# Kernel optimization log

Hardware: AMD Instinct MI355X
Metric: run time of the kernel (lower is better)

The kernel has to match this reference:

```python
import jax, jax.numpy as jnp
import numpy as np

HALF_PI = np.float32(np.pi / 2.0)
EPS = 1e-8

def feature_map(x):
    # [B, L] -> [B, L, 2]: standard quantum-inspired embedding
    return jnp.stack([jnp.cos(HALF_PI * x), jnp.sin(HALF_PI * x)], axis=-1)

def setup_inputs() -> dict:
    key = jax.random.key(0)
    k1, k2, k3, k4 = jax.random.split(key, 4)
    B, L, F, D, C = 32768, 256, 2, 32, 10
    x = jax.random.uniform(k1, (B, L), dtype=jnp.float32)
    core0 = jax.random.normal(k2, (F, 1, D), dtype=jnp.float32) * 0.1
    cores_mid = jax.random.normal(k3, (L - 2, F, D, D), dtype=jnp.float32) * 0.1
    coreN = jax.random.normal(k4, (F, D, C), dtype=jnp.float32) * 0.1
    return {"x": x, "core0": core0, "cores_mid": cores_mid, "coreN": coreN}

def reference(x, core0, cores_mid, coreN):
    feats = feature_map(x)                      # [B, L, F]
    # first site: M = v0 @ A0  -> [B, D]
    M0 = jnp.einsum('bf,fd->bd', feats[:, 0, :], core0[:, 0, :])

    # sequential scan over middle sites with per-step L2 normalization
    vs = jnp.transpose(feats[:, 1:-1, :], (1, 0, 2))  # [L-2, B, F]

    def step(M, inputs):
        v, A = inputs                           # v: [B,F], A: [F,D,D]
        M = jnp.einsum('ba,bf,fac->bc', M, v, A)
        M = M / (jnp.linalg.norm(M, axis=1, keepdims=True) + EPS)
        return M, None

    M, _ = jax.lax.scan(step, M0, (vs, cores_mid))

    # last site and readout
    final = jnp.einsum('bf,fac->bac', feats[:, -1, :], coreN)  # [B, D, C]
    logits = jnp.einsum('ba,bac->bc', M, final)                # [B, C]
    return logits
```

## Files before the change

kernel.cpp:

```cpp
#include <hip/hip_runtime.h>
#include <hip/hip_bf16.h>

#define B_TOTAL   32768
#define L_SITES   256
#define N_MID     254
#define HALF_PI_F 1.57079632679489662f
#define EPS_NORM  1e-8f

#define WS_FRAG 0
#define WS_C0   520192
#define WS_CN   520256
#define WS_X    520896
#define WS_FLAG 8909504

typedef short bf16x8 __attribute__((ext_vector_type(8)));
typedef float f32x4  __attribute__((ext_vector_type(4)));

__device__ __host__ __forceinline__ int pi_perm(int quad, int j) {
    return (j < 4) ? (quad * 4 + j) : (16 + quad * 4 + (j - 4));
}

__device__ __forceinline__ unsigned short f2bf(float f) {
    unsigned u = __builtin_bit_cast(unsigned, f);
    u += 0x7FFFu + ((u >> 16) & 1u);
    return (unsigned short)(u >> 16);
}
__device__ __forceinline__ float bf2f(unsigned short h) {
    unsigned u = ((unsigned)h) << 16;
    return __builtin_bit_cast(float, u);
}
__device__ __forceinline__ bf16x8 asbf(uint4 u) {
    return __builtin_bit_cast(bf16x8, u);
}
__device__ __forceinline__ unsigned pkbf2(float a, float b) {
    float2 p; p.x = a; p.y = b;
    __hip_bfloat162 h2 = __float22bfloat162_rn(p);
    unsigned u;
    __builtin_memcpy(&u, &h2, 4);
    return u;
}
__device__ __forceinline__ void split8(const float* v, bf16x8& hi, bf16x8& lo) {
    uint4 H, L;
    unsigned* hp = (unsigned*)&H;
    unsigned* lp = (unsigned*)&L;
    #pragma unroll
    for (int d = 0; d < 4; ++d) {
        float a = v[2 * d], b = v[2 * d + 1];
        unsigned hb = pkbf2(a, b);
        float h0 = __builtin_bit_cast(float, hb << 16);
        float h1 = __builtin_bit_cast(float, hb & 0xFFFF0000u);
        hp[d] = hb;
        lp[d] = pkbf2(a - h0, b - h1);
    }
    hi = __builtin_bit_cast(bf16x8, H);
    lo = __builtin_bit_cast(bf16x8, L);
}
__device__ __forceinline__ bool detect_bf16(const unsigned* x_raw, int lane) {
    unsigned v = x_raw[lane];
    return __ballot((v & 0xFFFFu) >= 0x4000u) == 0ull;
}

__global__ __launch_bounds__(256)
void aux_all(const void* __restrict__ x_in, const void* __restrict__ c0_in,
             const void* __restrict__ am_in, const void* __restrict__ cn_in,
             float* __restrict__ ws) {
    const int lane = threadIdx.x & 63;
    const bool bf = detect_bf16((const unsigned*)x_in, lane);
    const int b = blockIdx.x;

    if (b < 2048) {
        __shared__ float tile[64][65];
        const int bb = (b & 511) * 64;
        const int ll = (b >> 9) * 64;
        #pragma unroll
        for (int k = 0; k < 16; ++k) {
            int idx = threadIdx.x + k * 256;
            int row = idx >> 6, col = idx & 63;
            size_t gi = (size_t)(bb + row) * L_SITES + ll + col;
            float v = bf ? bf2f(((const unsigned short*)x_in)[gi])
                         : ((const float*)x_in)[gi];
            tile[row][col] = v;
        }
        __syncthreads();
        #pragma unroll
        for (int k = 0; k < 16; ++k) {
            int idx = threadIdx.x + k * 256;
            int row = idx >> 6, col = idx & 63;
            ws[WS_X + (size_t)(ll + row) * B_TOTAL + bb + col] = tile[col][row];
        }
    } else if (b < 2556) {
        int i = (b - 2048) * 256 + threadIdx.x;
        if (i < N_MID * 8 * 64) {
            const int l  = i & 63;
            const int q  = (i >> 6) & 7;
            const int t  = i >> 9;
            const int h  = q >> 2;
            const int kh = (q >> 1) & 1;
            const int p  = q & 1;
            const int m  = h * 16 + (l & 15);
            const int kb = (l >> 4) * 8;
            unsigned dw[4];
            #pragma unroll
            for (int d = 0; d < 4; ++d) {
                unsigned e01[2];
                #pragma unroll
                for (int s = 0; s < 2; ++s) {
                    int k  = kb + 2 * d + s;
                    int a  = pi_perm(k >> 3, k & 7);
                    size_t idx = ((size_t)(t * 2 + kh) * 32 + a) * 32 + m;
                    float v = bf ? bf2f(((const unsigned short*)am_in)[idx])
                                 : ((const float*)am_in)[idx];
                    unsigned short hi = f2bf(v);
                    e01[s] = (p == 0) ? hi : f2bf(v - bf2f(hi));
                }
                dw[d] = e01[0] | (e01[1] << 16);
            }
            uint4 o; o.x = dw[0]; o.y = dw[1]; o.z = dw[2]; o.w = dw[3];
            ((uint4*)ws)[(size_t)(t * 8 + q) * 64 + l] = o;
        }
    } else {
        for (int i = threadIdx.x; i < 640; i += 256) {
            if (i < 64)
                ws[WS_C0 + i] = bf ? bf2f(((const unsigned short*)c0_in)[i])
                                   : ((const float*)c0_in)[i];
            ws[WS_CN + i] = bf ? bf2f(((const unsigned short*)cn_in)[i])
                               : ((const float*)cn_in)[i];
        }
        if (threadIdx.x == 0)
            *(unsigned*)(ws + WS_FLAG) = bf ? 1u : 0u;
    }
}

__global__ __launch_bounds__(256)
void mps_mfma(const float* __restrict__ ws, void* __restrict__ out) {
    const int lane = threadIdx.x & 63;
    const int w    = threadIdx.x >> 6;
    const int r    = lane & 15;
    const int quad = lane >> 4;
    const int b0   = (blockIdx.x * 4 + w) * 16;
    const float* __restrict__ xT = ws + WS_X;
    const uint4* __restrict__ BF = (const uint4*)ws;
    const int i = b0 + r;

    float mm[8];
    {
        float x0 = xT[i];
        float sn, cs; __sincosf(HALF_PI_F * x0, &sn, &cs);
        const float* c0 = ws + WS_C0;
        #pragma unroll
        for (int j = 0; j < 8; ++j) {
            int a = pi_perm(quad, j);
            mm[j] = cs * c0[a] + sn * c0[32 + a];
        }
    }

#define DO_STEP(CT, ST, Q0, Q1, Q2, Q3, Q4, Q5, Q6, Q7, DONORM)                    \
    {                                                                              \
        float s0[8], s1[8];                                                        \
        _Pragma("unroll")                                                          \
        for (int j = 0; j < 8; ++j) { s0[j] = (CT) * mm[j]; s1[j] = (ST) * mm[j]; }\
        bf16x8 b0h, b0l, b1h, b1l;                                                 \
        split8(s0, b0h, b0l);                                                      \
        split8(s1, b1h, b1l);                                                      \
        const f32x4 z = {0.f, 0.f, 0.f, 0.f};                                      \
        __builtin_amdgcn_s_setprio(1);                                             \
        f32x4 a0 = __builtin_amdgcn_mfma_f32_16x16x32_bf16(asbf(Q0), b0h, z, 0, 0, 0);    \
        f32x4 a1 = __builtin_amdgcn_mfma_f32_16x16x32_bf16(asbf(Q4), b0h, z, 0, 0, 0);    \
        a0 = __builtin_amdgcn_mfma_f32_16x16x32_bf16(asbf(Q1), b0h, a0, 0, 0, 0);  \
        a1 = __builtin_amdgcn_mfma_f32_16x16x32_bf16(asbf(Q5), b0h, a1, 0, 0, 0);  \
        a0 = __builtin_amdgcn_mfma_f32_16x16x32_bf16(asbf(Q0), b0l, a0, 0, 0, 0);  \
        a1 = __builtin_amdgcn_mfma_f32_16x16x32_bf16(asbf(Q4), b0l, a1, 0, 0, 0);  \
        a0 = __builtin_amdgcn_mfma_f32_16x16x32_bf16(asbf(Q2), b1h, a0, 0, 0, 0);  \
        a1 = __builtin_amdgcn_mfma_f32_16x16x32_bf16(asbf(Q6), b1h, a1, 0, 0, 0);  \
        a0 = __builtin_amdgcn_mfma_f32_16x16x32_bf16(asbf(Q3), b1h, a0, 0, 0, 0);  \
        a1 = __builtin_amdgcn_mfma_f32_16x16x32_bf16(asbf(Q7), b1h, a1, 0, 0, 0);  \
        a0 = __builtin_amdgcn_mfma_f32_16x16x32_bf16(asbf(Q2), b1l, a0, 0, 0, 0);  \
        a1 = __builtin_amdgcn_mfma_f32_16x16x32_bf16(asbf(Q6), b1l, a1, 0, 0, 0);  \
        __builtin_amdgcn_s_setprio(0);                                             \
        mm[0] = a0[0]; mm[1] = a0[1]; mm[2] = a0[2]; mm[3] = a0[3];                \
        mm[4] = a1[0]; mm[5] = a1[1]; mm[6] = a1[2]; mm[7] = a1[3];                \
        if (DONORM) {                                                              \
            float ss = 0.f;                                                        \
            _Pragma("unroll")                                                      \
            for (int j = 0; j < 8; ++j) ss = fmaf(mm[j], mm[j], ss);               \
            ss += __shfl_xor(ss, 16);                                              \
            ss += __shfl_xor(ss, 32);                                              \
            float kk = 1.0f / (sqrtf(ss) + EPS_NORM);                              \
            _Pragma("unroll")                                                      \
            for (int j = 0; j < 8; ++j) mm[j] *= kk;                               \
        }                                                                          \
    }

    float ct0, st0;
    { float xc = xT[(size_t)B_TOTAL + i]; __sincosf(HALF_PI_F * xc, &st0, &ct0); }
    float x1 = xT[(size_t)2 * B_TOTAL + i];

    const uint4* Ba = BF + lane;
    uint4 fa0 = Ba[0],   fa1 = Ba[64],  fa2 = Ba[128], fa3 = Ba[192];
    uint4 fa4 = Ba[256], fa5 = Ba[320], fa6 = Ba[384], fa7 = Ba[448];

    #pragma unroll 1
    for (int t = 0; t < N_MID; t += 2) {
        const uint4* Bb = BF + (size_t)(t + 1) * 512 + lane;
        uint4 fb0 = Bb[0],   fb1 = Bb[64],  fb2 = Bb[128], fb3 = Bb[192];
        uint4 fb4 = Bb[256], fb5 = Bb[320], fb6 = Bb[384], fb7 = Bb[448];
        float x2 = xT[(size_t)(t + 3) * B_TOTAL + i];
        float ct1, st1; __sincosf(HALF_PI_F * x1, &st1, &ct1);

        DO_STEP(ct0, st0, fa0, fa1, fa2, fa3, fa4, fa5, fa6, fa7, false)

        const uint4* Bc = BF + (size_t)(t + 2) * 512 + lane;
        fa0 = Bc[0];   fa1 = Bc[64];  fa2 = Bc[128]; fa3 = Bc[192];
        fa4 = Bc[256]; fa5 = Bc[320]; fa6 = Bc[384]; fa7 = Bc[448];
        int xr = t + 4; if (xr > 255) xr = 255;
        x1 = xT[(size_t)xr * B_TOTAL + i];
        __sincosf(HALF_PI_F * x2, &st0, &ct0);

        DO_STEP(ct1, st1, fb0, fb1, fb2, fb3, fb4, fb5, fb6, fb7,
                (((t + 1) & 7) == 7) || (t + 1 == N_MID - 1))
    }
#undef DO_STEP

    {
        float xN = xT[(size_t)(L_SITES - 1) * B_TOTAL + i];
        float sN, cN; __sincosf(HALF_PI_F * xN, &sN, &cN);
        const float* kn = ws + WS_CN;
        float acc[10];
        #pragma unroll
        for (int c = 0; c < 10; ++c) acc[c] = 0.f;
        #pragma unroll
        for (int j = 0; j < 8; ++j) {
            int a = pi_perm(quad, j);
            float Ma = mm[j];
            #pragma unroll
            for (int c = 0; c < 10; ++c) {
                float fin = cN * kn[a * 10 + c] + sN * kn[320 + a * 10 + c];
                acc[c] = fmaf(Ma, fin, acc[c]);
            }
        }
        #pragma unroll
        for (int c = 0; c < 10; ++c) {
            acc[c] += __shfl_xor(acc[c], 16);
            acc[c] += __shfl_xor(acc[c], 32);
        }
        const unsigned bf = *(const unsigned*)(ws + WS_FLAG);
        if (quad == 0) {
            if (bf) {
                __hip_bfloat16* o = (__hip_bfloat16*)out;
                #pragma unroll
                for (int c = 0; c < 10; ++c)
                    o[(size_t)(b0 + r) * 10 + c] = __float2bfloat16(acc[c]);
            } else {
                float* o = (float*)out;
                #pragma unroll
                for (int c = 0; c < 10; ++c)
                    o[(size_t)(b0 + r) * 10 + c] = acc[c];
            }
        }
    }
}

extern "C" void kernel_launch(void* const* d_in, const int* in_sizes, int n_in,
                              void* d_out, int out_size, void* d_ws, size_t ws_size,
                              hipStream_t stream) {
    float* ws = (float*)d_ws;
    aux_all<<<2557, 256, 0, stream>>>(d_in[0], d_in[1], d_in[2], d_in[3], ws);
    mps_mfma<<<512, 256, 0, stream>>>(ws, d_out);
}
```

Measured before the change: 245.0 us.

## Factor feature scaling out of MFMA inputs and vectorize x transpose

The scan step now splits M into hi/lo bf16 once, runs separate MFMA chains for each feature's core, and combines them with cos/sin scaling in fp32 afterwards. This removes the per-step scaling and the second split, at the cost of four independent accumulator chains instead of two, which raises register use but exposes more MFMA parallelism. The aux transpose kernel also switches to float4/uint4 vector loads and stores to cut memory instruction count.

```diff
diff --git a/kernel.cpp b/kernel.cpp
--- a/kernel.cpp
+++ b/kernel.cpp
@@ -72,21 +72,47 @@
         __shared__ float tile[64][65];
         const int bb = (b & 511) * 64;
         const int ll = (b >> 9) * 64;
-        #pragma unroll
-        for (int k = 0; k < 16; ++k) {
-            int idx = threadIdx.x + k * 256;
-            int row = idx >> 6, col = idx & 63;
-            size_t gi = (size_t)(bb + row) * L_SITES + ll + col;
-            float v = bf ? bf2f(((const unsigned short*)x_in)[gi])
-                         : ((const float*)x_in)[gi];
-            tile[row][col] = v;
+        if (!bf) {
+            const float4* x4 = (const float4*)x_in;
+            const int tr = threadIdx.x >> 4;
+            const int q  = threadIdx.x & 15;
+            #pragma unroll
+            for (int u = 0; u < 4; ++u) {
+                int row = tr + u * 16;
+                float4 v = x4[(size_t)(bb + row) * (L_SITES / 4) + (ll / 4) + q];
+                tile[row][q * 4 + 0] = v.x;
+                tile[row][q * 4 + 1] = v.y;
+                tile[row][q * 4 + 2] = v.z;
+                tile[row][q * 4 + 3] = v.w;
+            }
+        } else {
+            const uint4* x8 = (const uint4*)x_in;
+            const int tr = threadIdx.x >> 3;
+            const int q  = threadIdx.x & 7;
+            #pragma unroll
+            for (int u = 0; u < 2; ++u) {
+                int row = tr + u * 32;
+                uint4 v = x8[(size_t)(bb + row) * (L_SITES / 8) + (ll / 8) + q];
+                const unsigned short* e = (const unsigned short*)&v;
+                #pragma unroll
+                for (int k = 0; k < 8; ++k) tile[row][q * 8 + k] = bf2f(e[k]);
+            }
         }
         __syncthreads();
-        #pragma unroll
-        for (int k = 0; k < 16; ++k) {
-            int idx = threadIdx.x + k * 256;
-            int row = idx >> 6, col = idx & 63;
-            ws[WS_X + (size_t)(ll + row) * B_TOTAL + bb + col] = tile[col][row];
+        {
+            const int tr = threadIdx.x >> 4;
+            const int q  = threadIdx.x & 15;
+            float4* o4 = (float4*)(ws + WS_X);
+            #pragma unroll
+            for (int u = 0; u < 4; ++u) {
+                int site = tr + u * 16;
+                float4 v;
+                v.x = tile[q * 4 + 0][site];
+                v.y = tile[q * 4 + 1][site];
+                v.z = tile[q * 4 + 2][site];
+                v.w = tile[q * 4 + 3][site];
+                o4[((size_t)(ll + site) * B_TOTAL + bb) / 4 + q] = v;
+            }
         }
     } else if (b < 2556) {
         int i = (b - 2048) * 256 + threadIdx.x;
@@ -156,29 +182,28 @@
 
 #define DO_STEP(CT, ST, Q0, Q1, Q2, Q3, Q4, Q5, Q6, Q7, DONORM)                    \
     {                                                                              \
-        float s0[8], s1[8];                                                        \
-        _Pragma("unroll")                                                          \
-        for (int j = 0; j < 8; ++j) { s0[j] = (CT) * mm[j]; s1[j] = (ST) * mm[j]; }\
-        bf16x8 b0h, b0l, b1h, b1l;                                                 \
-        split8(s0, b0h, b0l);                                                      \
-        split8(s1, b1h, b1l);                                                      \
+        bf16x8 mh, ml;                                                             \
+        split8(mm, mh, ml);                                                        \
         const f32x4 z = {0.f, 0.f, 0.f, 0.f};                                      \
         __builtin_amdgcn_s_setprio(1);                                             \
-        f32x4 a0 = __builtin_amdgcn_mfma_f32_16x16x32_bf16(asbf(Q0), b0h, z, 0, 0, 0);    \
-        f32x4 a1 = __builtin_amdgcn_mfma_f32_16x16x32_bf16(asbf(Q4), b0h, z, 0, 0, 0);    \
-        a0 = __builtin_amdgcn_mfma_f32_16x16x32_bf16(asbf(Q1), b0h, a0, 0, 0, 0);  \
-        a1 = __builtin_amdgcn_mfma_f32_16x16x32_bf16(asbf(Q5), b0h, a1, 0, 0, 0);  \
-        a0 = __builtin_amdgcn_mfma_f32_16x16x32_bf16(asbf(Q0), b0l, a0, 0, 0, 0);  \
-        a1 = __builtin_amdgcn_mfma_f32_16x16x32_bf16(asbf(Q4), b0l, a1, 0, 0, 0);  \
-        a0 = __builtin_amdgcn_mfma_f32_16x16x32_bf16(asbf(Q2), b1h, a0, 0, 0, 0);  \
-        a1 = __builtin_amdgcn_mfma_f32_16x16x32_bf16(asbf(Q6), b1h, a1, 0, 0, 0);  \
-        a0 = __builtin_amdgcn_mfma_f32_16x16x32_bf16(asbf(Q3), b1h, a0, 0, 0, 0);  \
-        a1 = __builtin_amdgcn_mfma_f32_16x16x32_bf16(asbf(Q7), b1h, a1, 0, 0, 0);  \
-        a0 = __builtin_amdgcn_mfma_f32_16x16x32_bf16(asbf(Q2), b1l, a0, 0, 0, 0);  \
-        a1 = __builtin_amdgcn_mfma_f32_16x16x32_bf16(asbf(Q6), b1l, a1, 0, 0, 0);  \
+        f32x4 p00 = __builtin_amdgcn_mfma_f32_16x16x32_bf16(asbf(Q0), mh, z, 0, 0, 0);    \
+        f32x4 p01 = __builtin_amdgcn_mfma_f32_16x16x32_bf16(asbf(Q2), mh, z, 0, 0, 0);    \
+        f32x4 p10 = __builtin_amdgcn_mfma_f32_16x16x32_bf16(asbf(Q4), mh, z, 0, 0, 0);    \
+        f32x4 p11 = __builtin_amdgcn_mfma_f32_16x16x32_bf16(asbf(Q6), mh, z, 0, 0, 0);    \
+        p00 = __builtin_amdgcn_mfma_f32_16x16x32_bf16(asbf(Q1), mh, p00, 0, 0, 0); \
+        p01 = __builtin_amdgcn_mfma_f32_16x16x32_bf16(asbf(Q3), mh, p01, 0, 0, 0); \
+        p10 = __builtin_amdgcn_mfma_f32_16x16x32_bf16(asbf(Q5), mh, p10, 0, 0, 0); \
+        p11 = __builtin_amdgcn_mfma_f32_16x16x32_bf16(asbf(Q7), mh, p11, 0, 0, 0); \
+        p00 = __builtin_amdgcn_mfma_f32_16x16x32_bf16(asbf(Q0), ml, p00, 0, 0, 0); \
+        p01 = __builtin_amdgcn_mfma_f32_16x16x32_bf16(asbf(Q2), ml, p01, 0, 0, 0); \
+        p10 = __builtin_amdgcn_mfma_f32_16x16x32_bf16(asbf(Q4), ml, p10, 0, 0, 0); \
+        p11 = __builtin_amdgcn_mfma_f32_16x16x32_bf16(asbf(Q6), ml, p11, 0, 0, 0); \
         __builtin_amdgcn_s_setprio(0);                                             \
-        mm[0] = a0[0]; mm[1] = a0[1]; mm[2] = a0[2]; mm[3] = a0[3];                \
-        mm[4] = a1[0]; mm[5] = a1[1]; mm[6] = a1[2]; mm[7] = a1[3];                \
+        _Pragma("unroll")                                                          \
+        for (int j = 0; j < 4; ++j) {                                              \
+            mm[j]     = fmaf((ST), p01[j], (CT) * p00[j]);                         \
+            mm[4 + j] = fmaf((ST), p11[j], (CT) * p10[j]);                         \
+        }                                                                          \
         if (DONORM) {                                                              \
             float ss = 0.f;                                                        \
             _Pragma("unroll")                                                      \
```

Result: faster. 232.9 us (-4.9%).
